# Kernel optimization log

Measured on AMD Instinct MI355X. Metric: run time of the kernel, lower is better.

## Reference

```python
import jax, jax.numpy as jnp
import numpy as np

NUM_HEADS = 16
EMBED = 1024
HEAD = EMBED // NUM_HEADS  # 64
MAX_DIST = 4
NEG_INF = -1e30


def setup_inputs() -> dict:
    key = jax.random.key(0)
    ks = jax.random.split(key, 8)
    B, S = 2, 2048
    x = jax.random.normal(ks[0], (B, S, EMBED), dtype=jnp.float32)
    return {
        "k": x,  # self-attention: k == v == q values
        "v": x,
        "q": x,
        "Wk": jax.random.normal(ks[1], (EMBED, EMBED), dtype=jnp.float32) * 0.02,
        "Wv": jax.random.normal(ks[2], (EMBED, EMBED), dtype=jnp.float32) * 0.02,
        "Wq": jax.random.normal(ks[3], (EMBED, EMBED), dtype=jnp.float32) * 0.02,
        "Wo": jax.random.normal(ks[4], (EMBED, EMBED), dtype=jnp.float32) * 0.02,
        "p_params": jax.random.normal(ks[5], (HEAD, 2 * MAX_DIST + 1), dtype=jnp.float32) * 0.02,
    }


def reference(k, v, q, Wk, Wv, Wq, Wo, p_params):
    B, Kl, _ = k.shape
    Ql = q.shape[1]
    # torch nn.Linear(bias=False): y = x @ W.T
    kh = (k @ Wk.T).reshape(B, Kl, NUM_HEADS, HEAD).transpose(0, 2, 1, 3)
    vh = (v @ Wv.T).reshape(B, Kl, NUM_HEADS, HEAD).transpose(0, 2, 1, 3)
    qh = (q @ Wq.T).reshape(B, Ql, NUM_HEADS, HEAD).transpose(0, 2, 1, 3)
    qh = qh / jnp.sqrt(jnp.float32(HEAD))
    # content scores: [B,H,Q,K]
    scores0 = jnp.einsum("bhqd,bhkd->bhqk", qh, kh)
    # relative-position bias: q . p_params[:, r] for each bucket r, then gather per (i,j)
    bias = jnp.einsum("bhqd,dr->bhqr", qh, p_params)  # [B,H,Q,2M+1]
    d = jnp.clip(jnp.arange(Ql)[:, None] - jnp.arange(Kl)[None, :], -MAX_DIST, MAX_DIST) + MAX_DIST  # [Q,K]
    rel = bias[:, :, jnp.arange(Ql)[:, None], d]  # [B,H,Q,K]
    scores = scores0 + rel
    # causal mask
    causal = jnp.arange(Ql)[:, None] >= jnp.arange(Kl)[None, :]
    scores = jnp.where(causal[None, None], scores, NEG_INF)
    attn = jax.nn.softmax(scores, axis=-1)
    out = jnp.einsum("bhqk,bhkd->bhqd", attn, vh)
    out = out.transpose(0, 2, 1, 3).reshape(B, Ql, EMBED)
    return out @ Wo.T
```

## Files before the change

kernel.cpp:

```cpp
#include <hip/hip_runtime.h>


using short8  = __attribute__((ext_vector_type(8))) short;
using floatx4 = __attribute__((ext_vector_type(4))) float;
using float4v = __attribute__((ext_vector_type(4))) float;
using ushort4v = __attribute__((ext_vector_type(4))) unsigned short;
using uint2v  = __attribute__((ext_vector_type(2))) unsigned int;

#define LOG2E 1.4426950408889634f

__device__ __forceinline__ unsigned short f2bf(float f) {
  unsigned u = __float_as_uint(f);
  return (unsigned short)((u + 0x7FFFu + ((u >> 16) & 1u)) >> 16);
}
__device__ __forceinline__ float bf2f(unsigned short s) {
  return __uint_as_float(((unsigned)s) << 16);
}
__device__ __forceinline__ unsigned cvt_pk_bf16(float lo, float hi) {
  unsigned r;
  asm("v_cvt_pk_bf16_f32 %0, %1, %2" : "=v"(r) : "v"(lo), "v"(hi));
  return r;
}
__device__ __forceinline__ void gload_lds16(const void* g, void* l) {
  __builtin_amdgcn_global_load_lds(
      (const __attribute__((address_space(1))) unsigned int*)g,
      (__attribute__((address_space(3))) unsigned int*)l, 16, 0, 0);
}

__global__ void f2bf_all(const float* __restrict__ x, unsigned short* xo,
                         const float* __restrict__ w0, unsigned short* o0,
                         const float* __restrict__ w1, unsigned short* o1,
                         const float* __restrict__ w2, unsigned short* o2,
                         const float* __restrict__ w3, unsigned short* o3) {
  int i = blockIdx.x * 256 + threadIdx.x;
  const float* in;
  unsigned short* out;
  int off;
  if (i < (1 << 20)) {
    in = x; out = xo; off = i;
  } else {
    int j = i - (1 << 20);
    int s = j >> 18;
    off = j & ((1 << 18) - 1);
    switch (s) {
      case 0: in = w0; out = o0; break;
      case 1: in = w1; out = o1; break;
      case 2: in = w2; out = o2; break;
      default: in = w3; out = o3; break;
    }
  }
  float4v v = ((const float4v*)in)[off];
  ushort4v o;
  o[0] = f2bf(v[0]); o[1] = f2bf(v[1]); o[2] = f2bf(v[2]); o[3] = f2bf(v[3]);
  ((ushort4v*)out)[off] = o;
}

template <int TM>
__device__ __forceinline__ void gemm_core64(
    const unsigned short* __restrict__ A, const unsigned short* __restrict__ B,
    void* __restrict__ Cv, int N, int K, int mBase, int nBase, float alpha,
    bool outbf, unsigned short* As, unsigned short* Bs) {
  const int tid = threadIdx.x;
  const int lane = tid & 63;
  const int w = tid >> 6;
  const int wr = w >> 1, wc = w & 1;
  const int lr = lane & 15, lg = lane >> 4;
  constexpr int NMF = TM / 32;

  floatx4 acc[NMF][4] = {};

  for (int k0 = 0; k0 < K; k0 += 64) {
#pragma unroll
    for (int i = 0; i < TM / 32; ++i) {
      int idx = i * 256 + tid;
      int row = idx >> 3, pc = idx & 7;
      int cl = pc ^ (row & 7);
      gload_lds16(A + (size_t)(mBase + row) * K + k0 + cl * 8, As + idx * 8);
    }
#pragma unroll
    for (int i = 0; i < 4; ++i) {
      int idx = i * 256 + tid;
      int row = idx >> 3, pc = idx & 7;
      int cl = pc ^ (row & 7);
      gload_lds16(B + (size_t)(nBase + row) * K + k0 + cl * 8, Bs + idx * 8);
    }
    __syncthreads();
#pragma unroll
    for (int c = 0; c < 2; ++c) {
      short8 af[NMF], bfr[4];
#pragma unroll
      for (int mf = 0; mf < NMF; ++mf) {
        int row = wr * (TM / 2) + mf * 16 + lr;
        af[mf] = *(const short8*)(As + row * 64 + (((c * 4 + lg) ^ (lr & 7)) * 8));
      }
#pragma unroll
      for (int nf = 0; nf < 4; ++nf) {
        int row = wc * 64 + nf * 16 + lr;
        bfr[nf] = *(const short8*)(Bs + row * 64 + (((c * 4 + lg) ^ (lr & 7)) * 8));
      }
#pragma unroll
      for (int mf = 0; mf < NMF; ++mf)
#pragma unroll
        for (int nf = 0; nf < 4; ++nf)
          acc[mf][nf] = __builtin_amdgcn_mfma_f32_16x16x32_bf16(
              af[mf], bfr[nf], acc[mf][nf], 0, 0, 0);
    }
    __syncthreads();
  }

#pragma unroll
  for (int mf = 0; mf < NMF; ++mf)
#pragma unroll
    for (int nf = 0; nf < 4; ++nf)
#pragma unroll
      for (int r = 0; r < 4; ++r) {
        size_t row = (size_t)mBase + wr * (TM / 2) + mf * 16 + lg * 4 + r;
        size_t col = (size_t)nBase + wc * 64 + nf * 16 + lr;
        float v = acc[mf][nf][r] * alpha;
        if (outbf)
          ((unsigned short*)Cv)[row * (size_t)N + col] = f2bf(v);
        else
          ((float*)Cv)[row * (size_t)N + col] = v;
      }
}

__global__ __launch_bounds__(256, 2) void proj3_kern(
    const unsigned short* __restrict__ xbf, const unsigned short* __restrict__ wkb,
    unsigned short* __restrict__ khb,
    const unsigned short* __restrict__ wqb, unsigned short* __restrict__ qhb,
    const unsigned short* __restrict__ wvb, unsigned short* __restrict__ vtb) {
  __shared__ alignas(16) unsigned short As[128 * 64];
  __shared__ alignas(16) unsigned short Bs[128 * 64];
  int z = blockIdx.z;
  if (z == 0)
    gemm_core64<128>(xbf, wkb, khb, 1024, 1024, blockIdx.y * 128,
                     blockIdx.x * 128, 1.0f, true, As, Bs);
  else if (z == 1)
    gemm_core64<128>(xbf, wqb, qhb, 1024, 1024, blockIdx.y * 128,
                     blockIdx.x * 128, 0.125f, true, As, Bs);
  else
    gemm_core64<128>(wvb, xbf, vtb, 4096, 1024, blockIdx.x * 128,
                     blockIdx.y * 128, 1.0f, true, As, Bs);
}

__global__ __launch_bounds__(256, 2) void gemm_out_kern(
    const unsigned short* __restrict__ A, const unsigned short* __restrict__ B,
    float* __restrict__ C) {
  __shared__ alignas(16) unsigned short As[64 * 64];
  __shared__ alignas(16) unsigned short Bs[128 * 64];
  gemm_core64<64>(A, B, C, 1024, 1024, blockIdx.y * 64, blockIdx.x * 128,
                  1.0f, false, As, Bs);
}

__global__ __launch_bounds__(256, 4) void attn_kern(
    const unsigned short* __restrict__ qh,
    const unsigned short* __restrict__ kh,
    const unsigned short* __restrict__ vt,
    const float* __restrict__ pp,
    unsigned short* __restrict__ ao,
    unsigned short* __restrict__ opart,
    float* __restrict__ mbuf,
    float* __restrict__ lbuf) {
  __shared__ alignas(16) char smem[40960];
  unsigned short* Qs  = (unsigned short*)smem;
  unsigned short* Vs1 = (unsigned short*)(smem + 8192);
  unsigned short* Ks0 = (unsigned short*)(smem + 16384);
  unsigned short* Vs0 = (unsigned short*)(smem + 24576);
  unsigned short* Ps  = (unsigned short*)(smem + 32768);
  float* ppS   = (float*)(smem + 32768);
  float* biasT = (float*)(smem + 35072);

  const int tid = threadIdx.x;
  const int lane = tid & 63;
  const int w = tid >> 6;
  const int lr = lane & 15, lg = lane >> 4;
  const int hb = blockIdx.x;
  const int h = hb & 15, b = hb >> 4;
  const int u = blockIdx.y;

  int qt, k0, k1;
  if (u == 0)       { qt = 15;     k0 = 0;  k1 = 16; }
  else if (u <= 16) { qt = 15 + u; k0 = 0;  k1 = 16; }
  else if (u == 17) { qt = 31;     k0 = 16; k1 = 32; }
  else {
    int p = (u - 18) >> 1;
    if (((u - 18) & 1) == 0) { qt = 14 - p; k0 = 0;  k1 = qt + 1; }
    else                     { qt = 30 - p; k0 = 16; k1 = qt + 1; }
  }
  const bool partial = (qt >= 16);
  const int qbase = qt * 64;
  const size_t bsQ = (size_t)b * 2048 + qbase;

  const unsigned short* khB = kh + ((size_t)b * 2048) * 1024 + h * 64;
  const unsigned short* vtB = vt + ((size_t)h * 64) * 4096 + b * 2048;

  auto stage_kv = [&](int kbase, unsigned short* Kd, unsigned short* Vd) {
#pragma unroll
    for (int i = 0; i < 2; ++i) {
      int idx = i * 256 + tid;
      int row = idx >> 3, pc = idx & 7;
      int cl = pc ^ (row & 7);
      gload_lds16(khB + ((size_t)(kbase + row) << 10) + cl * 8, Kd + idx * 8);
      gload_lds16(vtB + ((size_t)row << 12) + kbase + cl * 8, Vd + idx * 8);
    }
  };

#pragma unroll
  for (int i = 0; i < 2; ++i) {
    int idx = i * 256 + tid;
    int row = idx >> 3, c8 = (idx & 7) * 8;
    gload_lds16(qh + (bsQ + row) * 1024 + h * 64 + c8, Qs + idx * 8);
  }
  for (int idx = tid; idx < 576; idx += 256) {
    int r = idx >> 6, d = idx & 63;
    ppS[r * 64 + d] = pp[d * 9 + r];
  }
  stage_kv(k0 * 64, Ks0, Vs0);
  __syncthreads();

  const int qrowL = w * 16 + lr;
  short8 aq[2];
#pragma unroll
  for (int c = 0; c < 2; ++c)
    aq[c] = *(const short8*)(Qs + qrowL * 64 + c * 32 + lg * 8);

  for (int idx = tid; idx < 320; idx += 256) {
    int row = idx / 5, rr = idx - row * 5;
    const unsigned short* qrow = Qs + row * 64;
    const float* pr = ppS + (rr + 4) * 64;
    float s = 0.f;
#pragma unroll
    for (int d8 = 0; d8 < 8; ++d8) {
      short8 qv = *(const short8*)(qrow + d8 * 8);
#pragma unroll
      for (int j = 0; j < 8; ++j)
        s += bf2f((unsigned short)qv[j]) * pr[d8 * 8 + j];
    }
    biasT[row * 6 + rr] = s;
  }
  __syncthreads();

  const float b4 = biasT[qrowL * 6 + 0];
  const float b5 = biasT[qrowL * 6 + 1];
  const float b6 = biasT[qrowL * 6 + 2];
  const float b7 = biasT[qrowL * 6 + 3];
  const float b8 = biasT[qrowL * 6 + 4];
  __syncthreads();

  const int q_glob = qbase + w * 16 + lr;
  unsigned short* Pw = Ps + w * 1024;

  float m_run = -1e30f, l_run = 0.f;
  floatx4 o[4] = {};

  for (int kt = k0; kt < k1; ++kt) {
    const int kbase = kt * 64;
    const int cur = (kt - k0) & 1;
    unsigned short* Kc = cur ? Qs : Ks0;
    unsigned short* Vc = cur ? Vs1 : Vs0;
    if (kt + 1 < k1)
      stage_kv(kbase + 64, cur ? Ks0 : Qs, cur ? Vs0 : Vs1);

    floatx4 sa[4] = {};
    __builtin_amdgcn_s_setprio(1);
#pragma unroll
    for (int kf = 0; kf < 4; ++kf)
#pragma unroll
      for (int c = 0; c < 2; ++c) {
        int row = kf * 16 + lr;
        short8 ak = *(const short8*)(Kc + row * 64 +
                                     (((c * 4 + lg) ^ (lr & 7)) * 8));
        sa[kf] = __builtin_amdgcn_mfma_f32_16x16x32_bf16(ak, aq[c], sa[kf],
                                                         0, 0, 0);
      }
    __builtin_amdgcn_s_setprio(0);

    float bext;
    if (qbase + w * 16 >= kbase + 67) {
      bext = b8;
    } else {
      bext = 0.f;
#pragma unroll
      for (int kf = 0; kf < 4; ++kf)
#pragma unroll
        for (int r = 0; r < 4; ++r) {
          int dq = q_glob - (kbase + kf * 16 + lg * 4 + r);
          float bb = (dq >= 4) ? b8
                   : (dq == 0 ? b4 : (dq == 1 ? b5 : (dq == 2 ? b6 : b7)));
          sa[kf][r] = (dq < 0) ? -1e30f : (sa[kf][r] + bb);
        }
    }

    float mx = -1e30f;
#pragma unroll
    for (int kf = 0; kf < 4; ++kf)
#pragma unroll
      for (int r = 0; r < 4; ++r) mx = fmaxf(mx, sa[kf][r]);
    mx += bext;
    mx = fmaxf(mx, __shfl_xor(mx, 16, 64));
    mx = fmaxf(mx, __shfl_xor(mx, 32, 64));
    if (__any(mx > m_run + 8.f)) {
      float mn = fmaxf(m_run, mx);
      float al = __builtin_amdgcn_exp2f((m_run - mn) * LOG2E);
      m_run = mn;
      l_run *= al;
      float alo[4];
#pragma unroll
      for (int r = 0; r < 4; ++r) alo[r] = __shfl(al, lg * 4 + r, 64);
#pragma unroll
      for (int df = 0; df < 4; ++df)
#pragma unroll
        for (int r = 0; r < 4; ++r) o[df][r] *= alo[r];
    }

    const float c1 = (bext - m_run) * LOG2E;
    float rs = 0.f;
#pragma unroll
    for (int kf = 0; kf < 4; ++kf) {
      float p0 = __builtin_amdgcn_exp2f(fmaf(sa[kf][0], LOG2E, c1));
      float p1 = __builtin_amdgcn_exp2f(fmaf(sa[kf][1], LOG2E, c1));
      float p2 = __builtin_amdgcn_exp2f(fmaf(sa[kf][2], LOG2E, c1));
      float p3 = __builtin_amdgcn_exp2f(fmaf(sa[kf][3], LOG2E, c1));
      rs += (p0 + p1) + (p2 + p3);
      uint2v pk;
      pk[0] = cvt_pk_bf16(p0, p1);
      pk[1] = cvt_pk_bf16(p2, p3);
      int phys = (kf * 2 + (lg >> 1)) ^ (lr & 7);
      *(uint2v*)(Pw + lr * 64 + phys * 8 + (lg & 1) * 4) = pk;
    }
    rs += __shfl_xor(rs, 16, 64);
    rs += __shfl_xor(rs, 32, 64);
    l_run += rs;

    __builtin_amdgcn_s_setprio(1);
#pragma unroll
    for (int c = 0; c < 2; ++c) {
      short8 pa = *(const short8*)(Pw + lr * 64 +
                                   (((c * 4 + lg) ^ (lr & 7)) * 8));
#pragma unroll
      for (int df = 0; df < 4; ++df) {
        int row = df * 16 + lr;
        short8 bv = *(const short8*)(Vc + row * 64 +
                                     (((c * 4 + lg) ^ (lr & 7)) * 8));
        o[df] = __builtin_amdgcn_mfma_f32_16x16x32_bf16(pa, bv, o[df],
                                                        0, 0, 0);
      }
    }
    __builtin_amdgcn_s_setprio(0);
    __syncthreads();
  }

  if (!partial) {
    float rl[4];
#pragma unroll
    for (int r = 0; r < 4; ++r)
      rl[r] = __builtin_amdgcn_rcpf(__shfl(l_run, lg * 4 + r, 64));
    const size_t outRow0 = bsQ + w * 16 + lg * 4;
#pragma unroll
    for (int df = 0; df < 4; ++df)
#pragma unroll
      for (int r = 0; r < 4; ++r)
        ao[(outRow0 + r) * 1024 + h * 64 + df * 16 + lr] =
            f2bf(o[df][r] * rl[r]);
  } else {
    const int pid = (hb * 16 + (qt - 16)) * 2 + (k0 == 16 ? 1 : 0);
    unsigned short* op = opart + (size_t)pid * 4096;
#pragma unroll
    for (int df = 0; df < 4; ++df)
#pragma unroll
      for (int r = 0; r < 4; ++r)
        op[(w * 16 + lg * 4 + r) * 64 + df * 16 + lr] = f2bf(o[df][r]);
    if (lg == 0) {
      mbuf[pid * 64 + w * 16 + lr] = m_run;
      lbuf[pid * 64 + w * 16 + lr] = l_run;
    }
  }
}

__global__ void combine_kern(const unsigned short* __restrict__ opart,
                             const float* __restrict__ mbuf,
                             const float* __restrict__ lbuf,
                             unsigned short* __restrict__ ao) {
  const int t = blockIdx.x;
  const int hb = t >> 4;
  const int qtl = t & 15;
  const int qt = 16 + qtl;
  const int b = hb >> 4, h = hb & 15;
  const int pid0 = (hb * 16 + qtl) * 2, pid1 = pid0 + 1;
  const int row = threadIdx.x >> 2;
  const int colg = (threadIdx.x & 3) * 16;

  float m1 = mbuf[pid0 * 64 + row], m2 = mbuf[pid1 * 64 + row];
  float l1 = lbuf[pid0 * 64 + row], l2 = lbuf[pid1 * 64 + row];
  float m = fmaxf(m1, m2);
  float s1 = __builtin_amdgcn_exp2f((m1 - m) * LOG2E);
  float s2 = __builtin_amdgcn_exp2f((m2 - m) * LOG2E);
  float linv = 1.f / fmaf(l1, s1, l2 * s2);
  s1 *= linv; s2 *= linv;

  const unsigned short* O1 = opart + (size_t)pid0 * 4096 + row * 64 + colg;
  const unsigned short* O2 = opart + (size_t)pid1 * 4096 + row * 64 + colg;
  unsigned short* dst =
      ao + ((size_t)b * 2048 + qt * 64 + row) * 1024 + h * 64 + colg;
#pragma unroll
  for (int i = 0; i < 2; ++i) {
    short8 a = *(const short8*)(O1 + i * 8);
    short8 c = *(const short8*)(O2 + i * 8);
    short8 ov;
#pragma unroll
    for (int j = 0; j < 8; ++j)
      ov[j] = (short)f2bf(fmaf(bf2f((unsigned short)a[j]), s1,
                               bf2f((unsigned short)c[j]) * s2));
    *(short8*)(dst + i * 8) = ov;
  }
}

extern "C" void kernel_launch(void* const* d_in, const int* in_sizes, int n_in,
                              void* d_out, int out_size, void* d_ws,
                              size_t ws_size, hipStream_t stream) {
  const float* k_in = (const float*)d_in[0];
  const float* Wk = (const float*)d_in[3];
  const float* Wv = (const float*)d_in[4];
  const float* Wq = (const float*)d_in[5];
  const float* Wo = (const float*)d_in[6];
  const float* pp = (const float*)d_in[7];

  const size_t NX = 4096u * 1024u;
  const size_t NW = 1024u * 1024u;
  unsigned short* ws = (unsigned short*)d_ws;
  unsigned short* xbf = ws;
  unsigned short* wkb = xbf + NX;
  unsigned short* wvb = wkb + NW;
  unsigned short* wqb = wvb + NW;
  unsigned short* wob = wqb + NW;
  unsigned short* khb = wob + NW;
  unsigned short* vtb = khb + NX;
  unsigned short* qhb = vtb + NX;
  unsigned short* aob = qhb + NX;
  unsigned short* opart = aob + NX;
  float* mbuf = (float*)(opart + NX);
  float* lbuf = mbuf + 1024 * 64;

  (void)in_sizes; (void)n_in; (void)out_size; (void)ws_size;

  f2bf_all<<<dim3(8192), dim3(256), 0, stream>>>(
      k_in, xbf, Wk, wkb, Wv, wvb, Wq, wqb, Wo, wob);

  proj3_kern<<<dim3(8, 32, 3), dim3(256), 0, stream>>>(
      xbf, wkb, khb, wqb, qhb, wvb, vtb);

  attn_kern<<<dim3(32, 48), dim3(256), 0, stream>>>(qhb, khb, vtb, pp, aob,
                                                    opart, mbuf, lbuf);
  combine_kern<<<dim3(512), dim3(256), 0, stream>>>(opart, mbuf, lbuf, aob);

  gemm_out_kern<<<dim3(8, 64), dim3(256), 0, stream>>>(aob, wob, (float*)d_out);
}
```

Measured before the change: 104.9 us.

## Use 128-row query tiles with table-driven split-K work partition in attention

The attention kernel moves from 64-row query tiles with 256 threads to 128-row tiles with 512 threads (8 waves), so each staged K/V tile is shared by twice as many query rows. Work units come from a constant table that splits long query tiles into up to four key chunks. The combine kernel now merges 2–4 partials per row instead of exactly two. Waves whose rows lie entirely above the diagonal skip the MFMA and softmax work for that key tile but still join the barrier. The m/l buffers are placed in the dead xbf region, and the heavier per-block work and larger LDS may lower occupancy.

```diff
diff --git a/kernel.cpp b/kernel.cpp
--- a/kernel.cpp
+++ b/kernel.cpp
@@ -152,7 +152,23 @@
                   1.0f, false, As, Bs);
 }
 
-__global__ __launch_bounds__(256, 4) void attn_kern(
+#define ENC(qi, k0, k1, pp) ((qi) | ((k0) << 4) | ((k1) << 9) | ((pp) << 15))
+__device__ const unsigned int UTAB[38] = {
+    ENC(5, 0, 12, 63),  ENC(4, 0, 10, 63),  ENC(6, 0, 8, 0),
+    ENC(7, 0, 8, 2),    ENC(7, 8, 16, 3),   ENC(8, 0, 8, 4),
+    ENC(8, 8, 16, 5),   ENC(9, 0, 8, 7),    ENC(9, 8, 16, 8),
+    ENC(10, 0, 8, 10),  ENC(10, 8, 16, 11), ENC(11, 0, 8, 13),
+    ENC(11, 8, 16, 14), ENC(11, 16, 24, 15),ENC(12, 0, 8, 16),
+    ENC(12, 8, 16, 17), ENC(12, 16, 24, 18),ENC(13, 0, 8, 20),
+    ENC(13, 8, 16, 21), ENC(13, 16, 24, 22),ENC(14, 0, 8, 24),
+    ENC(14, 8, 16, 25), ENC(14, 16, 24, 26),ENC(15, 0, 8, 28),
+    ENC(15, 8, 16, 29), ENC(15, 16, 24, 30),ENC(15, 24, 32, 31),
+    ENC(3, 0, 8, 63),   ENC(2, 0, 6, 63),   ENC(6, 8, 14, 1),
+    ENC(10, 16, 22, 12),ENC(14, 24, 30, 27),ENC(1, 0, 4, 63),
+    ENC(9, 16, 20, 9),  ENC(13, 24, 28, 23),ENC(0, 0, 2, 63),
+    ENC(8, 16, 18, 6),  ENC(12, 24, 26, 19)};
+
+__global__ __launch_bounds__(512, 6) void attn_kern(
     const unsigned short* __restrict__ qh,
     const unsigned short* __restrict__ kh,
     const unsigned short* __restrict__ vt,
@@ -161,8 +177,9 @@
     unsigned short* __restrict__ opart,
     float* __restrict__ mbuf,
     float* __restrict__ lbuf) {
-  __shared__ alignas(16) char smem[40960];
-  unsigned short* Qs  = (unsigned short*)smem;
+  __shared__ alignas(16) char smem[49152];
+  unsigned short* QA  = (unsigned short*)smem;
+  unsigned short* Ks1 = (unsigned short*)smem;
   unsigned short* Vs1 = (unsigned short*)(smem + 8192);
   unsigned short* Ks0 = (unsigned short*)(smem + 16384);
   unsigned short* Vs0 = (unsigned short*)(smem + 24576);
@@ -176,57 +193,48 @@
   const int lr = lane & 15, lg = lane >> 4;
   const int hb = blockIdx.x;
   const int h = hb & 15, b = hb >> 4;
-  const int u = blockIdx.y;
-
-  int qt, k0, k1;
-  if (u == 0)       { qt = 15;     k0 = 0;  k1 = 16; }
-  else if (u <= 16) { qt = 15 + u; k0 = 0;  k1 = 16; }
-  else if (u == 17) { qt = 31;     k0 = 16; k1 = 32; }
-  else {
-    int p = (u - 18) >> 1;
-    if (((u - 18) & 1) == 0) { qt = 14 - p; k0 = 0;  k1 = qt + 1; }
-    else                     { qt = 30 - p; k0 = 16; k1 = qt + 1; }
-  }
-  const bool partial = (qt >= 16);
-  const int qbase = qt * 64;
+
+  const unsigned e = UTAB[blockIdx.y];
+  const int qi = e & 15;
+  const int k0t = (e >> 4) & 31;
+  const int k1t = (e >> 9) & 63;
+  const int pofs = (e >> 15) & 63;
+  const bool partial = (pofs != 63);
+  const int qbase = qi << 7;
   const size_t bsQ = (size_t)b * 2048 + qbase;
 
   const unsigned short* khB = kh + ((size_t)b * 2048) * 1024 + h * 64;
   const unsigned short* vtB = vt + ((size_t)h * 64) * 4096 + b * 2048;
 
   auto stage_kv = [&](int kbase, unsigned short* Kd, unsigned short* Vd) {
-#pragma unroll
-    for (int i = 0; i < 2; ++i) {
-      int idx = i * 256 + tid;
-      int row = idx >> 3, pc = idx & 7;
-      int cl = pc ^ (row & 7);
-      gload_lds16(khB + ((size_t)(kbase + row) << 10) + cl * 8, Kd + idx * 8);
-      gload_lds16(vtB + ((size_t)row << 12) + kbase + cl * 8, Vd + idx * 8);
-    }
+    int row = tid >> 3, pc = tid & 7;
+    int cl = pc ^ (row & 7);
+    gload_lds16(khB + ((size_t)(kbase + row) << 10) + cl * 8, Kd + tid * 8);
+    gload_lds16(vtB + ((size_t)row << 12) + kbase + cl * 8, Vd + tid * 8);
   };
 
 #pragma unroll
-  for (int i = 0; i < 2; ++i) {
-    int idx = i * 256 + tid;
+  for (int t = 0; t < 2; ++t) {
+    int idx = t * 512 + tid;
     int row = idx >> 3, c8 = (idx & 7) * 8;
-    gload_lds16(qh + (bsQ + row) * 1024 + h * 64 + c8, Qs + idx * 8);
-  }
-  for (int idx = tid; idx < 576; idx += 256) {
+    gload_lds16(qh + (bsQ + row) * 1024 + h * 64 + c8, QA + idx * 8);
+  }
+  for (int idx = tid; idx < 576; idx += 512) {
     int r = idx >> 6, d = idx & 63;
     ppS[r * 64 + d] = pp[d * 9 + r];
   }
-  stage_kv(k0 * 64, Ks0, Vs0);
+  stage_kv(k0t * 64, Ks0, Vs0);
   __syncthreads();
 
   const int qrowL = w * 16 + lr;
   short8 aq[2];
 #pragma unroll
   for (int c = 0; c < 2; ++c)
-    aq[c] = *(const short8*)(Qs + qrowL * 64 + c * 32 + lg * 8);
-
-  for (int idx = tid; idx < 320; idx += 256) {
+    aq[c] = *(const short8*)(QA + qrowL * 64 + c * 32 + lg * 8);
+
+  for (int idx = tid; idx < 640; idx += 512) {
     int row = idx / 5, rr = idx - row * 5;
-    const unsigned short* qrow = Qs + row * 64;
+    const unsigned short* qrow = QA + row * 64;
     const float* pr = ppS + (rr + 4) * 64;
     float s = 0.f;
 #pragma unroll
@@ -248,105 +256,108 @@
   __syncthreads();
 
   const int q_glob = qbase + w * 16 + lr;
+  const int wqtop = qbase + w * 16 + 15;
   unsigned short* Pw = Ps + w * 1024;
 
   float m_run = -1e30f, l_run = 0.f;
   floatx4 o[4] = {};
 
-  for (int kt = k0; kt < k1; ++kt) {
+  for (int kt = k0t; kt < k1t; ++kt) {
     const int kbase = kt * 64;
-    const int cur = (kt - k0) & 1;
-    unsigned short* Kc = cur ? Qs : Ks0;
+    const int cur = (kt - k0t) & 1;
+    unsigned short* Kc = cur ? Ks1 : Ks0;
     unsigned short* Vc = cur ? Vs1 : Vs0;
-    if (kt + 1 < k1)
-      stage_kv(kbase + 64, cur ? Ks0 : Qs, cur ? Vs0 : Vs1);
-
-    floatx4 sa[4] = {};
-    __builtin_amdgcn_s_setprio(1);
-#pragma unroll
-    for (int kf = 0; kf < 4; ++kf)
+    if (kt + 1 < k1t)
+      stage_kv(kbase + 64, cur ? Ks0 : Ks1, cur ? Vs0 : Vs1);
+
+    if (kbase <= wqtop) {
+      floatx4 sa[4] = {};
+      __builtin_amdgcn_s_setprio(1);
+#pragma unroll
+      for (int kf = 0; kf < 4; ++kf)
+#pragma unroll
+        for (int c = 0; c < 2; ++c) {
+          int row = kf * 16 + lr;
+          short8 ak = *(const short8*)(Kc + row * 64 +
+                                       (((c * 4 + lg) ^ (lr & 7)) * 8));
+          sa[kf] = __builtin_amdgcn_mfma_f32_16x16x32_bf16(ak, aq[c], sa[kf],
+                                                           0, 0, 0);
+        }
+      __builtin_amdgcn_s_setprio(0);
+
+      float bext;
+      if (qbase + w * 16 >= kbase + 67) {
+        bext = b8;
+      } else {
+        bext = 0.f;
+#pragma unroll
+        for (int kf = 0; kf < 4; ++kf)
+#pragma unroll
+          for (int r = 0; r < 4; ++r) {
+            int dq = q_glob - (kbase + kf * 16 + lg * 4 + r);
+            float bb = (dq >= 4) ? b8
+                     : (dq == 0 ? b4 : (dq == 1 ? b5 : (dq == 2 ? b6 : b7)));
+            sa[kf][r] = (dq < 0) ? -1e30f : (sa[kf][r] + bb);
+          }
+      }
+
+      float mx = -1e30f;
+#pragma unroll
+      for (int kf = 0; kf < 4; ++kf)
+#pragma unroll
+        for (int r = 0; r < 4; ++r) mx = fmaxf(mx, sa[kf][r]);
+      mx += bext;
+      mx = fmaxf(mx, __shfl_xor(mx, 16, 64));
+      mx = fmaxf(mx, __shfl_xor(mx, 32, 64));
+      if (__any(mx > m_run + 8.f)) {
+        float mn = fmaxf(m_run, mx);
+        float al = __builtin_amdgcn_exp2f((m_run - mn) * LOG2E);
+        m_run = mn;
+        l_run *= al;
+        float alo[4];
+#pragma unroll
+        for (int r = 0; r < 4; ++r) alo[r] = __shfl(al, lg * 4 + r, 64);
+#pragma unroll
+        for (int df = 0; df < 4; ++df)
+#pragma unroll
+          for (int r = 0; r < 4; ++r) o[df][r] *= alo[r];
+      }
+
+      const float c1 = (bext - m_run) * LOG2E;
+      float rs = 0.f;
+#pragma unroll
+      for (int kf = 0; kf < 4; ++kf) {
+        float p0 = __builtin_amdgcn_exp2f(fmaf(sa[kf][0], LOG2E, c1));
+        float p1 = __builtin_amdgcn_exp2f(fmaf(sa[kf][1], LOG2E, c1));
+        float p2 = __builtin_amdgcn_exp2f(fmaf(sa[kf][2], LOG2E, c1));
+        float p3 = __builtin_amdgcn_exp2f(fmaf(sa[kf][3], LOG2E, c1));
+        rs += (p0 + p1) + (p2 + p3);
+        uint2v pk;
+        pk[0] = cvt_pk_bf16(p0, p1);
+        pk[1] = cvt_pk_bf16(p2, p3);
+        int phys = (kf * 2 + (lg >> 1)) ^ (lr & 7);
+        *(uint2v*)(Pw + lr * 64 + phys * 8 + (lg & 1) * 4) = pk;
+      }
+      rs += __shfl_xor(rs, 16, 64);
+      rs += __shfl_xor(rs, 32, 64);
+      l_run += rs;
+
+      __builtin_amdgcn_s_setprio(1);
 #pragma unroll
       for (int c = 0; c < 2; ++c) {
-        int row = kf * 16 + lr;
-        short8 ak = *(const short8*)(Kc + row * 64 +
+        short8 pa = *(const short8*)(Pw + lr * 64 +
                                      (((c * 4 + lg) ^ (lr & 7)) * 8));
-        sa[kf] = __builtin_amdgcn_mfma_f32_16x16x32_bf16(ak, aq[c], sa[kf],
-                                                         0, 0, 0);
-      }
-    __builtin_amdgcn_s_setprio(0);
-
-    float bext;
-    if (qbase + w * 16 >= kbase + 67) {
-      bext = b8;
-    } else {
-      bext = 0.f;
-#pragma unroll
-      for (int kf = 0; kf < 4; ++kf)
-#pragma unroll
-        for (int r = 0; r < 4; ++r) {
-          int dq = q_glob - (kbase + kf * 16 + lg * 4 + r);
-          float bb = (dq >= 4) ? b8
-                   : (dq == 0 ? b4 : (dq == 1 ? b5 : (dq == 2 ? b6 : b7)));
-          sa[kf][r] = (dq < 0) ? -1e30f : (sa[kf][r] + bb);
+#pragma unroll
+        for (int df = 0; df < 4; ++df) {
+          int row = df * 16 + lr;
+          short8 bv = *(const short8*)(Vc + row * 64 +
+                                       (((c * 4 + lg) ^ (lr & 7)) * 8));
+          o[df] = __builtin_amdgcn_mfma_f32_16x16x32_bf16(pa, bv, o[df],
+                                                          0, 0, 0);
         }
-    }
-
-    float mx = -1e30f;
-#pragma unroll
-    for (int kf = 0; kf < 4; ++kf)
-#pragma unroll
-      for (int r = 0; r < 4; ++r) mx = fmaxf(mx, sa[kf][r]);
-    mx += bext;
-    mx = fmaxf(mx, __shfl_xor(mx, 16, 64));
-    mx = fmaxf(mx, __shfl_xor(mx, 32, 64));
-    if (__any(mx > m_run + 8.f)) {
-      float mn = fmaxf(m_run, mx);
-      float al = __builtin_amdgcn_exp2f((m_run - mn) * LOG2E);
-      m_run = mn;
-      l_run *= al;
-      float alo[4];
-#pragma unroll
-      for (int r = 0; r < 4; ++r) alo[r] = __shfl(al, lg * 4 + r, 64);
-#pragma unroll
-      for (int df = 0; df < 4; ++df)
-#pragma unroll
-        for (int r = 0; r < 4; ++r) o[df][r] *= alo[r];
-    }
-
-    const float c1 = (bext - m_run) * LOG2E;
-    float rs = 0.f;
-#pragma unroll
-    for (int kf = 0; kf < 4; ++kf) {
-      float p0 = __builtin_amdgcn_exp2f(fmaf(sa[kf][0], LOG2E, c1));
-      float p1 = __builtin_amdgcn_exp2f(fmaf(sa[kf][1], LOG2E, c1));
-      float p2 = __builtin_amdgcn_exp2f(fmaf(sa[kf][2], LOG2E, c1));
-      float p3 = __builtin_amdgcn_exp2f(fmaf(sa[kf][3], LOG2E, c1));
-      rs += (p0 + p1) + (p2 + p3);
-      uint2v pk;
-      pk[0] = cvt_pk_bf16(p0, p1);
-      pk[1] = cvt_pk_bf16(p2, p3);
-      int phys = (kf * 2 + (lg >> 1)) ^ (lr & 7);
-      *(uint2v*)(Pw + lr * 64 + phys * 8 + (lg & 1) * 4) = pk;
-    }
-    rs += __shfl_xor(rs, 16, 64);
-    rs += __shfl_xor(rs, 32, 64);
-    l_run += rs;
-
-    __builtin_amdgcn_s_setprio(1);
-#pragma unroll
-    for (int c = 0; c < 2; ++c) {
-      short8 pa = *(const short8*)(Pw + lr * 64 +
-                                   (((c * 4 + lg) ^ (lr & 7)) * 8));
-#pragma unroll
-      for (int df = 0; df < 4; ++df) {
-        int row = df * 16 + lr;
-        short8 bv = *(const short8*)(Vc + row * 64 +
-                                     (((c * 4 + lg) ^ (lr & 7)) * 8));
-        o[df] = __builtin_amdgcn_mfma_f32_16x16x32_bf16(pa, bv, o[df],
-                                                        0, 0, 0);
-      }
-    }
-    __builtin_amdgcn_s_setprio(0);
+      }
+      __builtin_amdgcn_s_setprio(0);
+    }
     __syncthreads();
   }
 
@@ -363,16 +374,16 @@
         ao[(outRow0 + r) * 1024 + h * 64 + df * 16 + lr] =
             f2bf(o[df][r] * rl[r]);
   } else {
-    const int pid = (hb * 16 + (qt - 16)) * 2 + (k0 == 16 ? 1 : 0);
-    unsigned short* op = opart + (size_t)pid * 4096;
+    const int pid = hb * 32 + pofs;
+    unsigned short* op = opart + (size_t)pid * 8192;
 #pragma unroll
     for (int df = 0; df < 4; ++df)
 #pragma unroll
       for (int r = 0; r < 4; ++r)
         op[(w * 16 + lg * 4 + r) * 64 + df * 16 + lr] = f2bf(o[df][r]);
     if (lg == 0) {
-      mbuf[pid * 64 + w * 16 + lr] = m_run;
-      lbuf[pid * 64 + w * 16 + lr] = l_run;
+      mbuf[pid * 128 + w * 16 + lr] = m_run;
+      lbuf[pid * 128 + w * 16 + lr] = l_run;
     }
   }
 }
@@ -381,37 +392,48 @@
                              const float* __restrict__ mbuf,
                              const float* __restrict__ lbuf,
                              unsigned short* __restrict__ ao) {
-  const int t = blockIdx.x;
-  const int hb = t >> 4;
-  const int qtl = t & 15;
-  const int qt = 16 + qtl;
+  const unsigned char NC[10] = {2, 2, 3, 3, 3, 3, 4, 4, 4, 4};
+  const unsigned char PB[10] = {0, 2, 4, 7, 10, 13, 16, 20, 24, 28};
+  const int bx = blockIdx.x;
+  const int hb = bx / 10, ii = bx - hb * 10;
+  const int i = 6 + ii;
   const int b = hb >> 4, h = hb & 15;
-  const int pid0 = (hb * 16 + qtl) * 2, pid1 = pid0 + 1;
-  const int row = threadIdx.x >> 2;
-  const int colg = (threadIdx.x & 3) * 16;
-
-  float m1 = mbuf[pid0 * 64 + row], m2 = mbuf[pid1 * 64 + row];
-  float l1 = lbuf[pid0 * 64 + row], l2 = lbuf[pid1 * 64 + row];
-  float m = fmaxf(m1, m2);
-  float s1 = __builtin_amdgcn_exp2f((m1 - m) * LOG2E);
-  float s2 = __builtin_amdgcn_exp2f((m2 - m) * LOG2E);
-  float linv = 1.f / fmaf(l1, s1, l2 * s2);
-  s1 *= linv; s2 *= linv;
-
-  const unsigned short* O1 = opart + (size_t)pid0 * 4096 + row * 64 + colg;
-  const unsigned short* O2 = opart + (size_t)pid1 * 4096 + row * 64 + colg;
+  const int nc = NC[ii];
+  const int pid0 = hb * 32 + PB[ii];
+  const int row = threadIdx.x >> 1;
+  const int colg = (threadIdx.x & 1) * 32;
+
+  float m[4], l[4];
+  float M = -1e30f;
+  for (int c = 0; c < nc; ++c) {
+    m[c] = mbuf[(pid0 + c) * 128 + row];
+    l[c] = lbuf[(pid0 + c) * 128 + row];
+    M = fmaxf(M, m[c]);
+  }
+  float s[4], lsum = 0.f;
+  for (int c = 0; c < nc; ++c) {
+    s[c] = __builtin_amdgcn_exp2f((m[c] - M) * LOG2E);
+    lsum = fmaf(l[c], s[c], lsum);
+  }
+  const float linv = 1.f / lsum;
+
   unsigned short* dst =
-      ao + ((size_t)b * 2048 + qt * 64 + row) * 1024 + h * 64 + colg;
-#pragma unroll
-  for (int i = 0; i < 2; ++i) {
-    short8 a = *(const short8*)(O1 + i * 8);
-    short8 c = *(const short8*)(O2 + i * 8);
+      ao + ((size_t)b * 2048 + i * 128 + row) * 1024 + h * 64 + colg;
+#pragma unroll
+  for (int t = 0; t < 4; ++t) {
+    float acc[8] = {};
+    for (int c = 0; c < nc; ++c) {
+      const unsigned short* Oc =
+          opart + (size_t)(pid0 + c) * 8192 + row * 64 + colg + t * 8;
+      short8 a = *(const short8*)Oc;
+#pragma unroll
+      for (int j = 0; j < 8; ++j)
+        acc[j] = fmaf(bf2f((unsigned short)a[j]), s[c], acc[j]);
+    }
     short8 ov;
 #pragma unroll
-    for (int j = 0; j < 8; ++j)
-      ov[j] = (short)f2bf(fmaf(bf2f((unsigned short)a[j]), s1,
-                               bf2f((unsigned short)c[j]) * s2));
-    *(short8*)(dst + i * 8) = ov;
+    for (int j = 0; j < 8; ++j) ov[j] = (short)f2bf(acc[j] * linv);
+    *(short8*)(dst + t * 8) = ov;
   }
 }
 
@@ -438,8 +460,8 @@
   unsigned short* qhb = vtb + NX;
   unsigned short* aob = qhb + NX;
   unsigned short* opart = aob + NX;
-  float* mbuf = (float*)(opart + NX);
-  float* lbuf = mbuf + 1024 * 64;
+  float* mbuf = (float*)xbf;
+  float* lbuf = mbuf + 1024 * 128;
 
   (void)in_sizes; (void)n_in; (void)out_size; (void)ws_size;
 
@@ -449,9 +471,9 @@
   proj3_kern<<<dim3(8, 32, 3), dim3(256), 0, stream>>>(
       xbf, wkb, khb, wqb, qhb, wvb, vtb);
 
-  attn_kern<<<dim3(32, 48), dim3(256), 0, stream>>>(qhb, khb, vtb, pp, aob,
+  attn_kern<<<dim3(32, 38), dim3(512), 0, stream>>>(qhb, khb, vtb, pp, aob,
                                                     opart, mbuf, lbuf);
-  combine_kern<<<dim3(512), dim3(256), 0, stream>>>(opart, mbuf, lbuf, aob);
+  combine_kern<<<dim3(320), dim3(256), 0, stream>>>(opart, mbuf, lbuf, aob);
 
   gemm_out_kern<<<dim3(8, 64), dim3(256), 0, stream>>>(aob, wob, (float*)d_out);
 }
```

New measurement: 145.5 us. 38.7% more time.

## Prefetch K/V tiles two steps ahead through registers instead of direct LDS loads

Applied to the files above, without the earlier changes.

Replaces direct global-to-LDS async loads for the next K/V tile with a register-staged pipeline. The tile two iterations ahead is loaded into registers while the next tile is written from registers into LDS. The end-of-iteration __syncthreads is replaced by an LDS-only waitcnt plus a raw barrier, so outstanding global loads need not drain at each barrier. This aims to hide global latency over a longer window, at the cost of extra VGPRs (four short8 per thread) and an explicit LDS write step. It relies on vmcnt being satisfied implicitly before the register-to-LDS writes.

```diff
diff --git a/kernel.cpp b/kernel.cpp
--- a/kernel.cpp
+++ b/kernel.cpp
@@ -194,15 +194,32 @@
   const unsigned short* khB = kh + ((size_t)b * 2048) * 1024 + h * 64;
   const unsigned short* vtB = vt + ((size_t)h * 64) * 4096 + b * 2048;
 
-  auto stage_kv = [&](int kbase, unsigned short* Kd, unsigned short* Vd) {
-#pragma unroll
-    for (int i = 0; i < 2; ++i) {
-      int idx = i * 256 + tid;
-      int row = idx >> 3, pc = idx & 7;
-      int cl = pc ^ (row & 7);
-      gload_lds16(khB + ((size_t)(kbase + row) << 10) + cl * 8, Kd + idx * 8);
-      gload_lds16(vtB + ((size_t)row << 12) + kbase + cl * 8, Vd + idx * 8);
-    }
+  const int srow0 = tid >> 3, spc = tid & 7;
+  const int scl0 = spc ^ (srow0 & 7);
+  const int srow1 = srow0 + 32;
+  const int scl1 = spc ^ (srow1 & 7);
+
+  auto stage_kv_lds = [&](int kbase, unsigned short* Kd, unsigned short* Vd) {
+    gload_lds16(khB + ((size_t)(kbase + srow0) << 10) + scl0 * 8, Kd + tid * 8);
+    gload_lds16(vtB + ((size_t)srow0 << 12) + kbase + scl0 * 8, Vd + tid * 8);
+    gload_lds16(khB + ((size_t)(kbase + srow1) << 10) + scl1 * 8,
+                Kd + (256 + tid) * 8);
+    gload_lds16(vtB + ((size_t)srow1 << 12) + kbase + scl1 * 8,
+                Vd + (256 + tid) * 8);
+  };
+
+  short8 kreg0, kreg1, vreg0, vreg1;
+  auto load_regs = [&](int kbase) {
+    kreg0 = *(const short8*)(khB + ((size_t)(kbase + srow0) << 10) + scl0 * 8);
+    vreg0 = *(const short8*)(vtB + ((size_t)srow0 << 12) + kbase + scl0 * 8);
+    kreg1 = *(const short8*)(khB + ((size_t)(kbase + srow1) << 10) + scl1 * 8);
+    vreg1 = *(const short8*)(vtB + ((size_t)srow1 << 12) + kbase + scl1 * 8);
+  };
+  auto write_regs = [&](unsigned short* Kd, unsigned short* Vd) {
+    *(short8*)(Kd + tid * 8) = kreg0;
+    *(short8*)(Vd + tid * 8) = vreg0;
+    *(short8*)(Kd + (256 + tid) * 8) = kreg1;
+    *(short8*)(Vd + (256 + tid) * 8) = vreg1;
   };
 
 #pragma unroll
@@ -215,7 +232,7 @@
     int r = idx >> 6, d = idx & 63;
     ppS[r * 64 + d] = pp[d * 9 + r];
   }
-  stage_kv(k0 * 64, Ks0, Vs0);
+  stage_kv_lds(k0 * 64, Ks0, Vs0);
   __syncthreads();
 
   const int qrowL = w * 16 + lr;
@@ -250,6 +267,8 @@
   const int q_glob = qbase + w * 16 + lr;
   unsigned short* Pw = Ps + w * 1024;
 
+  if (k0 + 1 < k1) load_regs((k0 + 1) * 64);
+
   float m_run = -1e30f, l_run = 0.f;
   floatx4 o[4] = {};
 
@@ -258,8 +277,9 @@
     const int cur = (kt - k0) & 1;
     unsigned short* Kc = cur ? Qs : Ks0;
     unsigned short* Vc = cur ? Vs1 : Vs0;
-    if (kt + 1 < k1)
-      stage_kv(kbase + 64, cur ? Ks0 : Qs, cur ? Vs0 : Vs1);
+
+    if (kt + 1 < k1) write_regs(cur ? Ks0 : Qs, cur ? Vs0 : Vs1);
+    if (kt + 2 < k1) load_regs((kbase + 128));
 
     floatx4 sa[4] = {};
     __builtin_amdgcn_s_setprio(1);
@@ -347,7 +367,9 @@
       }
     }
     __builtin_amdgcn_s_setprio(0);
-    __syncthreads();
+
+    asm volatile("s_waitcnt lgkmcnt(0)" ::: "memory");
+    __builtin_amdgcn_s_barrier();
   }
 
   if (!partial) {
```

After: 102.1 us, median of 2. 1.03x faster.
